# Optimization experiments

Measured on AMD Instinct MI355X. Metric: run time of the kernel, lower is better.

Reference implementation:

```python
import jax, jax.numpy as jnp
import numpy as np

K = 2  # kernel_size == stride, padding=0, dilation=1 -> non-overlapping 2x2x2 blocks


def setup_inputs() -> dict:
    key = jax.random.key(0)
    # (b, c, s, w, h) volumetric batch
    x = jax.random.normal(key, (8, 1, 64, 192, 192), dtype=jnp.float32)
    return {"x": x}


def _extract_blocks(x, k):
    # Faithful to extract_patches_3d with stride==kernel, padding=0, dilation=1:
    # the double unfold + permute + flat view yields rows ordered (b, c, do, ho, wo),
    # each row the flattened k*k*k patch.
    b, c, s, w, h = x.shape
    blk = x.reshape(b, c, s // k, k, w // k, k, h // k, k)
    blk = blk.transpose(0, 1, 2, 4, 6, 3, 5, 7)  # (b,c,do,ho,wo,k,k,k)
    return blk.reshape(-1, k * k * k)  # (N, k^3)


def reference(x):
    b, c, s, w, h = x.shape
    data = _extract_blocks(x, K)            # (N, 8)
    mean = jnp.mean(data, axis=0)           # (8,)
    centered = data - mean
    # torch.svd: data = U S V^T ; jax returns vh = V^T
    _, _, vh = jnp.linalg.svd(centered, full_matrices=False)
    pca_components = vh[:1].T               # (8, n_components=1)
    reduced = centered @ pca_components     # (N, 1)
    out = reduced.reshape(b, c, s // K, w // K, h // K)
    return out, mean, pca_components
```

## Files before the change

kernel.cpp:

```cpp
#include <hip/hip_runtime.h>

constexpr int NB     = 8 * 32 * 96 * 96;
constexpr int NPAIR  = NB / 2;
constexpr int NACC   = 44;
constexpr int GRID_A = 1024;
constexpr int TPB    = 256;
constexpr int GRID_P = 2048;

__global__ __launch_bounds__(TPB, 4)
void reduce_kernel(const float* __restrict__ x, float* __restrict__ partials,
                   unsigned int* __restrict__ ctr) {
  if (blockIdx.x == 0 && threadIdx.x == 0) *ctr = 0u;

  float acc[NACC];
#pragma unroll
  for (int i = 0; i < NACC; ++i) acc[i] = 0.0f;

  int tid = blockIdx.x * TPB + threadIdx.x;
  const int stride = GRID_A * TPB;
  for (int p = tid; p < NPAIR; p += stride) {
    int hp = p % 48;
    int t1 = p / 48;
    int wo = t1 % 96;
    int t2 = t1 / 96;
    int so = t2 % 32;
    int b  = t2 / 32;
    const float* base = x + (((b * 64 + 2 * so) * 192 + 2 * wo) * 192 + 4 * hp);
    float4 r0 = *(const float4*)(base);
    float4 r1 = *(const float4*)(base + 192);
    float4 r2 = *(const float4*)(base + 192 * 192);
    float4 r3 = *(const float4*)(base + 192 * 192 + 192);
    float v0[8] = {r0.x, r0.y, r1.x, r1.y, r2.x, r2.y, r3.x, r3.y};
    float v1[8] = {r0.z, r0.w, r1.z, r1.w, r2.z, r2.w, r3.z, r3.w};
#pragma unroll
    for (int a = 0; a < 8; ++a) acc[a] += v0[a] + v1[a];
    int k = 8;
#pragma unroll
    for (int a = 0; a < 8; ++a)
#pragma unroll
      for (int q = a; q < 8; ++q) acc[k++] += v0[a] * v0[q] + v1[a] * v1[q];
  }

#pragma unroll
  for (int i = 0; i < NACC; ++i) {
    float v = acc[i];
    for (int off = 32; off >= 1; off >>= 1) v += __shfl_down(v, off, 64);
    acc[i] = v;
  }
  __shared__ float lds[4][NACC];
  int lane = threadIdx.x & 63;
  int wv   = threadIdx.x >> 6;
  if (lane == 0) {
#pragma unroll
    for (int i = 0; i < NACC; ++i) lds[wv][i] = acc[i];
  }
  __syncthreads();
  if (threadIdx.x < NACC) {
    float s = lds[0][threadIdx.x] + lds[1][threadIdx.x] +
              lds[2][threadIdx.x] + lds[3][threadIdx.x];
    partials[threadIdx.x * GRID_A + blockIdx.x] = s;
  }
}

__device__ __forceinline__ float rdlane(float x, int lane) {
  return __int_as_float(__builtin_amdgcn_readlane(__float_as_int(x), lane));
}

template <int P, int Q>
__device__ __forceinline__ void jrot(const float (&r)[8], float& ct, float& st) {
  float app = rdlane(r[P], P);
  float aqq = rdlane(r[Q], Q);
  float apq = rdlane(r[Q], P);
  float theta = (aqq - app) * 0.5f * __builtin_amdgcn_rcpf(apq);
  float root  = __builtin_amdgcn_sqrtf(theta * theta + 1.0f);
  float tmag  = __builtin_amdgcn_rcpf(fabsf(theta) + root);
  float tt    = copysignf(tmag, theta);
  float c     = __builtin_amdgcn_rsqf(tt * tt + 1.0f);
  float s     = tt * c;
  bool zero   = (apq == 0.0f);
  ct = zero ? 1.0f : c;
  st = zero ? 0.0f : s;
}

template <int P, int Q>
__device__ __forceinline__ void jcol(float (&r)[8], float (&v)[8], float c, float s) {
  float rp = r[P], rq = r[Q];
  r[P] = c * rp - s * rq;
  r[Q] = s * rp + c * rq;
  float vp = v[P], vq = v[Q];
  v[P] = c * vp - s * vq;
  v[Q] = s * vp + c * vq;
}

template <int P0,int Q0,int P1,int Q1,int P2,int Q2,int P3,int Q3>
__device__ __forceinline__ void jacobi_round(float (&r)[8], float (&v)[8], int i) {
  float c0,s0,c1,s1,c2,s2,c3,s3;
  jrot<P0,Q0>(r, c0, s0);
  jrot<P1,Q1>(r, c1, s1);
  jrot<P2,Q2>(r, c2, s2);
  jrot<P3,Q3>(r, c3, s3);
  jcol<P0,Q0>(r, v, c0, s0);
  jcol<P1,Q1>(r, v, c1, s1);
  jcol<P2,Q2>(r, v, c2, s2);
  jcol<P3,Q3>(r, v, c3, s3);
  float alpha = 1.0f, beta = 0.0f;
  int plane = i;
  if (i == P0) { alpha = c0; beta = -s0; plane = Q0; }
  if (i == Q0) { alpha = c0; beta =  s0; plane = P0; }
  if (i == P1) { alpha = c1; beta = -s1; plane = Q1; }
  if (i == Q1) { alpha = c1; beta =  s1; plane = P1; }
  if (i == P2) { alpha = c2; beta = -s2; plane = Q2; }
  if (i == Q2) { alpha = c2; beta =  s2; plane = P2; }
  if (i == P3) { alpha = c3; beta = -s3; plane = Q3; }
  if (i == Q3) { alpha = c3; beta =  s3; plane = P3; }
  float prow[8];
#pragma unroll
  for (int j = 0; j < 8; ++j) prow[j] = __shfl(r[j], plane, 64);
#pragma unroll
  for (int j = 0; j < 8; ++j) r[j] = alpha * r[j] + beta * prow[j];
}

__global__ __launch_bounds__(TPB)
void mid_solve_kernel(const float* __restrict__ partials, double* __restrict__ sums_d,
                      unsigned int* __restrict__ ctr, float* __restrict__ res,
                      float* __restrict__ out_tail) {
  int a = blockIdx.x;
  int t = threadIdx.x;
  const float* row = partials + a * GRID_A;
  double s = (double)row[t] + (double)row[t + 256] +
             (double)row[t + 512] + (double)row[t + 768];
  for (int off = 32; off >= 1; off >>= 1) s += __shfl_down(s, off, 64);
  __shared__ double lds[4];
  __shared__ bool is_last;
  if ((t & 63) == 0) lds[t >> 6] = s;
  __syncthreads();
  if (t == 0) {
    sums_d[a] = lds[0] + lds[1] + lds[2] + lds[3];
    __threadfence();
    unsigned int old = atomicAdd(ctr, 1u);
    is_last = (old == (unsigned int)(NACC - 1));
  }
  __syncthreads();
  if (!is_last) return;
  __threadfence();

  __shared__ double sums[NACC];
  if (t < NACC) sums[t] = sums_d[t];
  __syncthreads();
  if (t >= 64) return;

  const int i = t & 7;
  const double invN = 1.0 / (double)NB;
  double mean[8];
#pragma unroll
  for (int j = 0; j < 8; ++j) mean[j] = sums[j] * invN;

  double mean_i = mean[0];
#pragma unroll
  for (int k = 1; k < 8; ++k) if (i == k) mean_i = mean[k];

  double rowd[8];
#pragma unroll
  for (int j = 0; j < 8; ++j) {
    int p = i < j ? i : j;
    int q = i < j ? j : i;
    int idx = 8 + p * 8 - (p * (p - 1)) / 2 + (q - p);
    rowd[j] = sums[idx] - (double)NB * mean_i * mean[j];
  }
  double tr = 0.0;
#pragma unroll
  for (int k = 0; k < 8; ++k) tr += __shfl(rowd[k], k, 64);
  double shift = tr * 0.125;

  float r[8], v[8];
#pragma unroll
  for (int j = 0; j < 8; ++j) {
    double d = rowd[j] - (j == i ? shift : 0.0);
    r[j] = (float)(d * (1.0 / 1536.0));
    v[j] = (j == i) ? 1.0f : 0.0f;
  }

#pragma unroll 1
  for (int sweep = 0; sweep < 6; ++sweep) {
    jacobi_round<7,0, 1,6, 2,5, 3,4>(r, v, i);
    jacobi_round<7,1, 2,0, 3,6, 4,5>(r, v, i);
    jacobi_round<7,2, 3,1, 4,0, 5,6>(r, v, i);
    jacobi_round<7,3, 4,2, 5,1, 6,0>(r, v, i);
    jacobi_round<7,4, 5,3, 6,2, 0,1>(r, v, i);
    jacobi_round<7,5, 6,4, 0,3, 1,2>(r, v, i);
    jacobi_round<7,6, 0,5, 1,4, 2,3>(r, v, i);
  }

  float diag[8];
#pragma unroll
  for (int k = 0; k < 8; ++k) diag[k] = rdlane(r[k], k);
  int best = 0; float bd = diag[0];
#pragma unroll
  for (int k = 1; k < 8; ++k) if (diag[k] > bd) { bd = diag[k]; best = k; }
  float vi = v[0];
#pragma unroll
  for (int k = 1; k < 8; ++k) if (best == k) vi = v[k];
  float vec[8];
#pragma unroll
  for (int k = 0; k < 8; ++k) vec[k] = rdlane(vi, k);
  float nrm2 = 0.0f;
#pragma unroll
  for (int k = 0; k < 8; ++k) nrm2 += vec[k] * vec[k];
  float inv = 1.0f / sqrtf(nrm2);
#pragma unroll
  for (int k = 0; k < 8; ++k) vec[k] *= inv;
  int m = 0; float am = fabsf(vec[0]);
#pragma unroll
  for (int k = 1; k < 8; ++k) { float aa = fabsf(vec[k]); if (aa > am) { am = aa; m = k; } }
  float vm = vec[0];
#pragma unroll
  for (int k = 1; k < 8; ++k) if (m == k) vm = vec[k];
  if (vm > 0.0f) {
#pragma unroll
    for (int k = 0; k < 8; ++k) vec[k] = -vec[k];
  }
  double c0d = 0.0;
#pragma unroll
  for (int k = 0; k < 8; ++k) c0d += mean[k] * (double)vec[k];

  float mi = (float)mean[0];
#pragma unroll
  for (int k = 1; k < 8; ++k) if (i == k) mi = (float)mean[k];
  float vl = vec[0];
#pragma unroll
  for (int k = 1; k < 8; ++k) if (i == k) vl = vec[k];

  if (t < 8) {
    res[t]            = vl;
    out_tail[t]       = mi;
    out_tail[8 + t]   = vl;
  }
  if (t == 0) res[8] = (float)c0d;
}

__global__ __launch_bounds__(TPB, 8)
void project_kernel(const float* __restrict__ x, const float* __restrict__ res,
                    float* __restrict__ out) {
  __shared__ float s_res[9];
  if (threadIdx.x < 9) s_res[threadIdx.x] = res[threadIdx.x];
  __syncthreads();
  float w0 = s_res[0], w1 = s_res[1], w2 = s_res[2], w3 = s_res[3];
  float w4 = s_res[4], w5 = s_res[5], w6 = s_res[6], w7 = s_res[7];
  float c0 = s_res[8];
  float2* out2 = (float2*)out;
  const int stride = GRID_P * TPB;
  for (int p = blockIdx.x * TPB + threadIdx.x; p < NPAIR; p += stride) {
    int hp = p % 48;
    int t1 = p / 48;
    int wo = t1 % 96;
    int t2 = t1 / 96;
    int so = t2 % 32;
    int b  = t2 / 32;
    const float* base = x + (((b * 64 + 2 * so) * 192 + 2 * wo) * 192 + 4 * hp);
    float4 r0 = *(const float4*)(base);
    float4 r1 = *(const float4*)(base + 192);
    float4 r2 = *(const float4*)(base + 192 * 192);
    float4 r3 = *(const float4*)(base + 192 * 192 + 192);
    float o0 = r0.x * w0 + r0.y * w1 + r1.x * w2 + r1.y * w3
             + r2.x * w4 + r2.y * w5 + r3.x * w6 + r3.y * w7 - c0;
    float o1 = r0.z * w0 + r0.w * w1 + r1.z * w2 + r1.w * w3
             + r2.z * w4 + r2.w * w5 + r3.z * w6 + r3.w * w7 - c0;
    out2[p] = make_float2(o0, o1);
  }
}

extern "C" void kernel_launch(void* const* d_in, const int* in_sizes, int n_in,
                              void* d_out, int out_size, void* d_ws, size_t ws_size,
                              hipStream_t stream) {
  (void)in_sizes; (void)n_in; (void)out_size; (void)ws_size;
  const float* x = (const float*)d_in[0];
  float* out = (float*)d_out;
  float* partials      = (float*)d_ws;
  double* sums_d       = (double*)(partials + NACC * GRID_A);
  float* res           = (float*)(sums_d + NACC);
  unsigned int* ctr    = (unsigned int*)(res + 16);

  reduce_kernel<<<GRID_A, TPB, 0, stream>>>(x, partials, ctr);
  mid_solve_kernel<<<NACC, TPB, 0, stream>>>(partials, sums_d, ctr, res, out + NB);
  project_kernel<<<GRID_P, TPB, 0, stream>>>(x, res, out);
}
```

Measured before the change: 63.59 us.

## Fuse eigen-solve into projection kernel via flag spin-wait, widen per-thread work

Merges the mid-level reduction/Jacobi solve kernel into the projection kernel. The first NACC blocks do the final sums and the last one solves the eigenproblem and sets a release flag, while every block spin-waits on that flag before projecting. This removes one kernel launch. Both the reduce and project loops now handle four blocks per thread using eight float4 loads and a float4 store, and the projection grid is halved. The spin-wait relies on all solver blocks being co-resident with the waiting blocks. With 1024 blocks at 4 per CU this is likely but not guaranteed, so there is some deadlock risk.

```diff
diff --git a/kernel.cpp b/kernel.cpp
--- a/kernel.cpp
+++ b/kernel.cpp
@@ -1,16 +1,16 @@
 #include <hip/hip_runtime.h>
 
 constexpr int NB     = 8 * 32 * 96 * 96;
-constexpr int NPAIR  = NB / 2;
+constexpr int NQUAD  = NB / 4;
 constexpr int NACC   = 44;
 constexpr int GRID_A = 1024;
 constexpr int TPB    = 256;
-constexpr int GRID_P = 2048;
+constexpr int GRID_P = 1024;
 
 __global__ __launch_bounds__(TPB, 4)
 void reduce_kernel(const float* __restrict__ x, float* __restrict__ partials,
-                   unsigned int* __restrict__ ctr) {
-  if (blockIdx.x == 0 && threadIdx.x == 0) *ctr = 0u;
+                   unsigned int* __restrict__ ctr, unsigned int* __restrict__ flag) {
+  if (blockIdx.x == 0 && threadIdx.x == 0) { *ctr = 0u; *flag = 0u; }
 
   float acc[NACC];
 #pragma unroll
@@ -18,27 +18,41 @@
 
   int tid = blockIdx.x * TPB + threadIdx.x;
   const int stride = GRID_A * TPB;
-  for (int p = tid; p < NPAIR; p += stride) {
-    int hp = p % 48;
-    int t1 = p / 48;
+  for (int q = tid; q < NQUAD; q += stride) {
+    int hq = q % 24;
+    int t1 = q / 24;
     int wo = t1 % 96;
     int t2 = t1 / 96;
     int so = t2 % 32;
     int b  = t2 / 32;
-    const float* base = x + (((b * 64 + 2 * so) * 192 + 2 * wo) * 192 + 4 * hp);
-    float4 r0 = *(const float4*)(base);
-    float4 r1 = *(const float4*)(base + 192);
-    float4 r2 = *(const float4*)(base + 192 * 192);
-    float4 r3 = *(const float4*)(base + 192 * 192 + 192);
-    float v0[8] = {r0.x, r0.y, r1.x, r1.y, r2.x, r2.y, r3.x, r3.y};
-    float v1[8] = {r0.z, r0.w, r1.z, r1.w, r2.z, r2.w, r3.z, r3.w};
-#pragma unroll
-    for (int a = 0; a < 8; ++a) acc[a] += v0[a] + v1[a];
+    const float* base = x + (((b * 64 + 2 * so) * 192 + 2 * wo) * 192 + 8 * hq);
+    float4 a0 = *(const float4*)(base);
+    float4 b0 = *(const float4*)(base + 4);
+    float4 a1 = *(const float4*)(base + 192);
+    float4 b1 = *(const float4*)(base + 196);
+    float4 a2 = *(const float4*)(base + 192 * 192);
+    float4 b2 = *(const float4*)(base + 192 * 192 + 4);
+    float4 a3 = *(const float4*)(base + 192 * 192 + 192);
+    float4 b3 = *(const float4*)(base + 192 * 192 + 196);
+    float P[4][8] = {
+      {a0.x, a0.y, a1.x, a1.y, a2.x, a2.y, a3.x, a3.y},
+      {a0.z, a0.w, a1.z, a1.w, a2.z, a2.w, a3.z, a3.w},
+      {b0.x, b0.y, b1.x, b1.y, b2.x, b2.y, b3.x, b3.y},
+      {b0.z, b0.w, b1.z, b1.w, b2.z, b2.w, b3.z, b3.w}};
+#pragma unroll
+    for (int a = 0; a < 8; ++a)
+      acc[a] += (P[0][a] + P[1][a]) + (P[2][a] + P[3][a]);
     int k = 8;
 #pragma unroll
     for (int a = 0; a < 8; ++a)
 #pragma unroll
-      for (int q = a; q < 8; ++q) acc[k++] += v0[a] * v0[q] + v1[a] * v1[q];
+      for (int c = a; c < 8; ++c) {
+        float t = P[0][a] * P[0][c];
+        t += P[1][a] * P[1][c];
+        t += P[2][a] * P[2][c];
+        t += P[3][a] * P[3][c];
+        acc[k++] += t;
+      }
   }
 
 #pragma unroll
@@ -120,152 +134,169 @@
   for (int j = 0; j < 8; ++j) r[j] = alpha * r[j] + beta * prow[j];
 }
 
-__global__ __launch_bounds__(TPB)
-void mid_solve_kernel(const float* __restrict__ partials, double* __restrict__ sums_d,
-                      unsigned int* __restrict__ ctr, float* __restrict__ res,
-                      float* __restrict__ out_tail) {
-  int a = blockIdx.x;
+__global__ __launch_bounds__(TPB, 4)
+void project_solve_kernel(const float* __restrict__ x,
+                          const float* __restrict__ partials,
+                          double* __restrict__ sums_d,
+                          unsigned int* __restrict__ ctr,
+                          unsigned int* __restrict__ flag,
+                          float* __restrict__ res,
+                          float* __restrict__ out,
+                          float* __restrict__ out_tail) {
   int t = threadIdx.x;
-  const float* row = partials + a * GRID_A;
-  double s = (double)row[t] + (double)row[t + 256] +
-             (double)row[t + 512] + (double)row[t + 768];
-  for (int off = 32; off >= 1; off >>= 1) s += __shfl_down(s, off, 64);
-  __shared__ double lds[4];
-  __shared__ bool is_last;
-  if ((t & 63) == 0) lds[t >> 6] = s;
+
+  if (blockIdx.x < NACC) {
+    const float* row = partials + blockIdx.x * GRID_A;
+    float4 u = ((const float4*)row)[t];
+    double s = (double)u.x + (double)u.y + (double)u.z + (double)u.w;
+    for (int off = 32; off >= 1; off >>= 1) s += __shfl_down(s, off, 64);
+    __shared__ double ldsd[4];
+    __shared__ bool is_last;
+    if ((t & 63) == 0) ldsd[t >> 6] = s;
+    __syncthreads();
+    if (t == 0) {
+      sums_d[blockIdx.x] = ldsd[0] + ldsd[1] + ldsd[2] + ldsd[3];
+      __threadfence();
+      unsigned int old = atomicAdd(ctr, 1u);
+      is_last = (old == (unsigned int)(NACC - 1));
+    }
+    __syncthreads();
+    if (is_last) {
+      __threadfence();
+      __shared__ double sums[NACC];
+      if (t < NACC) sums[t] = sums_d[t];
+      __syncthreads();
+      if (t < 64) {
+        const int i = t & 7;
+        const double invN = 1.0 / (double)NB;
+        double mean[8];
+#pragma unroll
+        for (int j = 0; j < 8; ++j) mean[j] = sums[j] * invN;
+        double mean_i = mean[0];
+#pragma unroll
+        for (int k = 1; k < 8; ++k) if (i == k) mean_i = mean[k];
+        double rowd[8];
+#pragma unroll
+        for (int j = 0; j < 8; ++j) {
+          int p = i < j ? i : j;
+          int q = i < j ? j : i;
+          int idx = 8 + p * 8 - (p * (p - 1)) / 2 + (q - p);
+          rowd[j] = sums[idx] - (double)NB * mean_i * mean[j];
+        }
+        double tr = 0.0;
+#pragma unroll
+        for (int k = 0; k < 8; ++k) tr += __shfl(rowd[k], k, 64);
+        double shift = tr * 0.125;
+
+        float r[8], v[8];
+#pragma unroll
+        for (int j = 0; j < 8; ++j) {
+          double d = rowd[j] - (j == i ? shift : 0.0);
+          r[j] = (float)(d * (1.0 / 1536.0));
+          v[j] = (j == i) ? 1.0f : 0.0f;
+        }
+#pragma unroll 1
+        for (int sweep = 0; sweep < 6; ++sweep) {
+          jacobi_round<7,0, 1,6, 2,5, 3,4>(r, v, i);
+          jacobi_round<7,1, 2,0, 3,6, 4,5>(r, v, i);
+          jacobi_round<7,2, 3,1, 4,0, 5,6>(r, v, i);
+          jacobi_round<7,3, 4,2, 5,1, 6,0>(r, v, i);
+          jacobi_round<7,4, 5,3, 6,2, 0,1>(r, v, i);
+          jacobi_round<7,5, 6,4, 0,3, 1,2>(r, v, i);
+          jacobi_round<7,6, 0,5, 1,4, 2,3>(r, v, i);
+        }
+        float diag[8];
+#pragma unroll
+        for (int k = 0; k < 8; ++k) diag[k] = rdlane(r[k], k);
+        int best = 0; float bd = diag[0];
+#pragma unroll
+        for (int k = 1; k < 8; ++k) if (diag[k] > bd) { bd = diag[k]; best = k; }
+        float vi = v[0];
+#pragma unroll
+        for (int k = 1; k < 8; ++k) if (best == k) vi = v[k];
+        float vec[8];
+#pragma unroll
+        for (int k = 0; k < 8; ++k) vec[k] = rdlane(vi, k);
+        float nrm2 = 0.0f;
+#pragma unroll
+        for (int k = 0; k < 8; ++k) nrm2 += vec[k] * vec[k];
+        float inv = 1.0f / sqrtf(nrm2);
+#pragma unroll
+        for (int k = 0; k < 8; ++k) vec[k] *= inv;
+        int m = 0; float am = fabsf(vec[0]);
+#pragma unroll
+        for (int k = 1; k < 8; ++k) { float aa = fabsf(vec[k]); if (aa > am) { am = aa; m = k; } }
+        float vm = vec[0];
+#pragma unroll
+        for (int k = 1; k < 8; ++k) if (m == k) vm = vec[k];
+        if (vm > 0.0f) {
+#pragma unroll
+          for (int k = 0; k < 8; ++k) vec[k] = -vec[k];
+        }
+        double c0d = 0.0;
+#pragma unroll
+        for (int k = 0; k < 8; ++k) c0d += mean[k] * (double)vec[k];
+        float mi = (float)mean[0];
+#pragma unroll
+        for (int k = 1; k < 8; ++k) if (i == k) mi = (float)mean[k];
+        float vl = vec[0];
+#pragma unroll
+        for (int k = 1; k < 8; ++k) if (i == k) vl = vec[k];
+        if (t < 8) {
+          res[t]          = vl;
+          out_tail[t]     = mi;
+          out_tail[8 + t] = vl;
+        }
+        if (t == 0) res[8] = (float)c0d;
+      }
+      __syncthreads();
+      if (t == 0) {
+        __threadfence();
+        __hip_atomic_store(flag, 1u, __ATOMIC_RELEASE, __HIP_MEMORY_SCOPE_AGENT);
+      }
+    }
+  }
+
+  __shared__ float s_res[9];
+  if (t == 0) {
+    while (__hip_atomic_load(flag, __ATOMIC_ACQUIRE, __HIP_MEMORY_SCOPE_AGENT) == 0u)
+      __builtin_amdgcn_s_sleep(2);
+  }
   __syncthreads();
-  if (t == 0) {
-    sums_d[a] = lds[0] + lds[1] + lds[2] + lds[3];
-    __threadfence();
-    unsigned int old = atomicAdd(ctr, 1u);
-    is_last = (old == (unsigned int)(NACC - 1));
-  }
+  if (t < 9)
+    s_res[t] = __hip_atomic_load(&res[t], __ATOMIC_RELAXED, __HIP_MEMORY_SCOPE_AGENT);
   __syncthreads();
-  if (!is_last) return;
-  __threadfence();
-
-  __shared__ double sums[NACC];
-  if (t < NACC) sums[t] = sums_d[t];
-  __syncthreads();
-  if (t >= 64) return;
-
-  const int i = t & 7;
-  const double invN = 1.0 / (double)NB;
-  double mean[8];
-#pragma unroll
-  for (int j = 0; j < 8; ++j) mean[j] = sums[j] * invN;
-
-  double mean_i = mean[0];
-#pragma unroll
-  for (int k = 1; k < 8; ++k) if (i == k) mean_i = mean[k];
-
-  double rowd[8];
-#pragma unroll
-  for (int j = 0; j < 8; ++j) {
-    int p = i < j ? i : j;
-    int q = i < j ? j : i;
-    int idx = 8 + p * 8 - (p * (p - 1)) / 2 + (q - p);
-    rowd[j] = sums[idx] - (double)NB * mean_i * mean[j];
-  }
-  double tr = 0.0;
-#pragma unroll
-  for (int k = 0; k < 8; ++k) tr += __shfl(rowd[k], k, 64);
-  double shift = tr * 0.125;
-
-  float r[8], v[8];
-#pragma unroll
-  for (int j = 0; j < 8; ++j) {
-    double d = rowd[j] - (j == i ? shift : 0.0);
-    r[j] = (float)(d * (1.0 / 1536.0));
-    v[j] = (j == i) ? 1.0f : 0.0f;
-  }
-
-#pragma unroll 1
-  for (int sweep = 0; sweep < 6; ++sweep) {
-    jacobi_round<7,0, 1,6, 2,5, 3,4>(r, v, i);
-    jacobi_round<7,1, 2,0, 3,6, 4,5>(r, v, i);
-    jacobi_round<7,2, 3,1, 4,0, 5,6>(r, v, i);
-    jacobi_round<7,3, 4,2, 5,1, 6,0>(r, v, i);
-    jacobi_round<7,4, 5,3, 6,2, 0,1>(r, v, i);
-    jacobi_round<7,5, 6,4, 0,3, 1,2>(r, v, i);
-    jacobi_round<7,6, 0,5, 1,4, 2,3>(r, v, i);
-  }
-
-  float diag[8];
-#pragma unroll
-  for (int k = 0; k < 8; ++k) diag[k] = rdlane(r[k], k);
-  int best = 0; float bd = diag[0];
-#pragma unroll
-  for (int k = 1; k < 8; ++k) if (diag[k] > bd) { bd = diag[k]; best = k; }
-  float vi = v[0];
-#pragma unroll
-  for (int k = 1; k < 8; ++k) if (best == k) vi = v[k];
-  float vec[8];
-#pragma unroll
-  for (int k = 0; k < 8; ++k) vec[k] = rdlane(vi, k);
-  float nrm2 = 0.0f;
-#pragma unroll
-  for (int k = 0; k < 8; ++k) nrm2 += vec[k] * vec[k];
-  float inv = 1.0f / sqrtf(nrm2);
-#pragma unroll
-  for (int k = 0; k < 8; ++k) vec[k] *= inv;
-  int m = 0; float am = fabsf(vec[0]);
-#pragma unroll
-  for (int k = 1; k < 8; ++k) { float aa = fabsf(vec[k]); if (aa > am) { am = aa; m = k; } }
-  float vm = vec[0];
-#pragma unroll
-  for (int k = 1; k < 8; ++k) if (m == k) vm = vec[k];
-  if (vm > 0.0f) {
-#pragma unroll
-    for (int k = 0; k < 8; ++k) vec[k] = -vec[k];
-  }
-  double c0d = 0.0;
-#pragma unroll
-  for (int k = 0; k < 8; ++k) c0d += mean[k] * (double)vec[k];
-
-  float mi = (float)mean[0];
-#pragma unroll
-  for (int k = 1; k < 8; ++k) if (i == k) mi = (float)mean[k];
-  float vl = vec[0];
-#pragma unroll
-  for (int k = 1; k < 8; ++k) if (i == k) vl = vec[k];
-
-  if (t < 8) {
-    res[t]            = vl;
-    out_tail[t]       = mi;
-    out_tail[8 + t]   = vl;
-  }
-  if (t == 0) res[8] = (float)c0d;
-}
-
-__global__ __launch_bounds__(TPB, 8)
-void project_kernel(const float* __restrict__ x, const float* __restrict__ res,
-                    float* __restrict__ out) {
-  __shared__ float s_res[9];
-  if (threadIdx.x < 9) s_res[threadIdx.x] = res[threadIdx.x];
-  __syncthreads();
+
   float w0 = s_res[0], w1 = s_res[1], w2 = s_res[2], w3 = s_res[3];
   float w4 = s_res[4], w5 = s_res[5], w6 = s_res[6], w7 = s_res[7];
   float c0 = s_res[8];
-  float2* out2 = (float2*)out;
+  float4* out4 = (float4*)out;
   const int stride = GRID_P * TPB;
-  for (int p = blockIdx.x * TPB + threadIdx.x; p < NPAIR; p += stride) {
-    int hp = p % 48;
-    int t1 = p / 48;
+  for (int q = blockIdx.x * TPB + t; q < NQUAD; q += stride) {
+    int hq = q % 24;
+    int t1 = q / 24;
     int wo = t1 % 96;
     int t2 = t1 / 96;
     int so = t2 % 32;
     int b  = t2 / 32;
-    const float* base = x + (((b * 64 + 2 * so) * 192 + 2 * wo) * 192 + 4 * hp);
-    float4 r0 = *(const float4*)(base);
-    float4 r1 = *(const float4*)(base + 192);
-    float4 r2 = *(const float4*)(base + 192 * 192);
-    float4 r3 = *(const float4*)(base + 192 * 192 + 192);
-    float o0 = r0.x * w0 + r0.y * w1 + r1.x * w2 + r1.y * w3
-             + r2.x * w4 + r2.y * w5 + r3.x * w6 + r3.y * w7 - c0;
-    float o1 = r0.z * w0 + r0.w * w1 + r1.z * w2 + r1.w * w3
-             + r2.z * w4 + r2.w * w5 + r3.z * w6 + r3.w * w7 - c0;
-    out2[p] = make_float2(o0, o1);
+    const float* base = x + (((b * 64 + 2 * so) * 192 + 2 * wo) * 192 + 8 * hq);
+    float4 a0 = *(const float4*)(base);
+    float4 b0 = *(const float4*)(base + 4);
+    float4 a1 = *(const float4*)(base + 192);
+    float4 b1 = *(const float4*)(base + 196);
+    float4 a2 = *(const float4*)(base + 192 * 192);
+    float4 b2 = *(const float4*)(base + 192 * 192 + 4);
+    float4 a3 = *(const float4*)(base + 192 * 192 + 192);
+    float4 b3 = *(const float4*)(base + 192 * 192 + 196);
+    float o0 = a0.x * w0 + a0.y * w1 + a1.x * w2 + a1.y * w3
+             + a2.x * w4 + a2.y * w5 + a3.x * w6 + a3.y * w7 - c0;
+    float o1 = a0.z * w0 + a0.w * w1 + a1.z * w2 + a1.w * w3
+             + a2.z * w4 + a2.w * w5 + a3.z * w6 + a3.w * w7 - c0;
+    float o2 = b0.x * w0 + b0.y * w1 + b1.x * w2 + b1.y * w3
+             + b2.x * w4 + b2.y * w5 + b3.x * w6 + b3.y * w7 - c0;
+    float o3 = b0.z * w0 + b0.w * w1 + b1.z * w2 + b1.w * w3
+             + b2.z * w4 + b2.w * w5 + b3.z * w6 + b3.w * w7 - c0;
+    out4[q] = make_float4(o0, o1, o2, o3);
   }
 }
 
@@ -275,12 +306,13 @@
   (void)in_sizes; (void)n_in; (void)out_size; (void)ws_size;
   const float* x = (const float*)d_in[0];
   float* out = (float*)d_out;
-  float* partials      = (float*)d_ws;
-  double* sums_d       = (double*)(partials + NACC * GRID_A);
-  float* res           = (float*)(sums_d + NACC);
-  unsigned int* ctr    = (unsigned int*)(res + 16);
-
-  reduce_kernel<<<GRID_A, TPB, 0, stream>>>(x, partials, ctr);
-  mid_solve_kernel<<<NACC, TPB, 0, stream>>>(partials, sums_d, ctr, res, out + NB);
-  project_kernel<<<GRID_P, TPB, 0, stream>>>(x, res, out);
-}
+  float* partials   = (float*)d_ws;
+  double* sums_d    = (double*)(partials + NACC * GRID_A);
+  float* res        = (float*)(sums_d + NACC);
+  unsigned int* ctr = (unsigned int*)(res + 16);
+  unsigned int* flg = ctr + 1;
+
+  reduce_kernel<<<GRID_A, TPB, 0, stream>>>(x, partials, ctr, flg);
+  project_solve_kernel<<<GRID_P, TPB, 0, stream>>>(x, partials, sums_d, ctr, flg,
+                                                   res, out, out + NB);
+}
```

Result: slower. 119.9 us (+88.6%).

## Fuse mid-reduction and eigen-solve into projection kernel with flag spin-wait

Applied to the files above, without the earlier changes.

Removes the separate mid_solve launch by having the first NACC blocks of the projection kernel reduce partials and, via the last-block counter, run the Jacobi eigen-solve. It then publishes the results with a release-ordered flag. All projection blocks spin on the flag before reading the weights. This aims to save a kernel launch and inter-kernel gap, at the cost of relying on co-residency of the solver blocks to avoid deadlock and on busy-waiting.

```diff
diff --git a/kernel.cpp b/kernel.cpp
--- a/kernel.cpp
+++ b/kernel.cpp
@@ -9,8 +9,8 @@
 
 __global__ __launch_bounds__(TPB, 4)
 void reduce_kernel(const float* __restrict__ x, float* __restrict__ partials,
-                   unsigned int* __restrict__ ctr) {
-  if (blockIdx.x == 0 && threadIdx.x == 0) *ctr = 0u;
+                   unsigned int* __restrict__ ctr, unsigned int* __restrict__ flag) {
+  if (blockIdx.x == 0 && threadIdx.x == 0) { *ctr = 0u; *flag = 0u; }
 
   float acc[NACC];
 #pragma unroll
@@ -120,136 +120,145 @@
   for (int j = 0; j < 8; ++j) r[j] = alpha * r[j] + beta * prow[j];
 }
 
-__global__ __launch_bounds__(TPB)
-void mid_solve_kernel(const float* __restrict__ partials, double* __restrict__ sums_d,
-                      unsigned int* __restrict__ ctr, float* __restrict__ res,
-                      float* __restrict__ out_tail) {
-  int a = blockIdx.x;
+__global__ __launch_bounds__(TPB, 8)
+void project_solve_kernel(const float* __restrict__ x,
+                          const float* __restrict__ partials,
+                          double* __restrict__ sums_d,
+                          unsigned int* __restrict__ ctr,
+                          unsigned int* __restrict__ flag,
+                          float* __restrict__ res,
+                          float* __restrict__ out,
+                          float* __restrict__ out_tail) {
   int t = threadIdx.x;
-  const float* row = partials + a * GRID_A;
-  double s = (double)row[t] + (double)row[t + 256] +
-             (double)row[t + 512] + (double)row[t + 768];
-  for (int off = 32; off >= 1; off >>= 1) s += __shfl_down(s, off, 64);
-  __shared__ double lds[4];
-  __shared__ bool is_last;
-  if ((t & 63) == 0) lds[t >> 6] = s;
+
+  if (blockIdx.x < NACC) {
+    const float* row = partials + blockIdx.x * GRID_A;
+    float4 u = ((const float4*)row)[t];
+    double s = (double)u.x + (double)u.y + (double)u.z + (double)u.w;
+    for (int off = 32; off >= 1; off >>= 1) s += __shfl_down(s, off, 64);
+    __shared__ double ldsd[4];
+    __shared__ bool is_last;
+    if ((t & 63) == 0) ldsd[t >> 6] = s;
+    __syncthreads();
+    if (t == 0) {
+      sums_d[blockIdx.x] = ldsd[0] + ldsd[1] + ldsd[2] + ldsd[3];
+      __threadfence();
+      unsigned int old = atomicAdd(ctr, 1u);
+      is_last = (old == (unsigned int)(NACC - 1));
+    }
+    __syncthreads();
+    if (is_last) {
+      __threadfence();
+      __shared__ double sums[NACC];
+      if (t < NACC) sums[t] = sums_d[t];
+      __syncthreads();
+      if (t < 64) {
+        const int i = t & 7;
+        const double invN = 1.0 / (double)NB;
+        double mean[8];
+#pragma unroll
+        for (int j = 0; j < 8; ++j) mean[j] = sums[j] * invN;
+        double mean_i = mean[0];
+#pragma unroll
+        for (int k = 1; k < 8; ++k) if (i == k) mean_i = mean[k];
+        double rowd[8];
+#pragma unroll
+        for (int j = 0; j < 8; ++j) {
+          int p = i < j ? i : j;
+          int q = i < j ? j : i;
+          int idx = 8 + p * 8 - (p * (p - 1)) / 2 + (q - p);
+          rowd[j] = sums[idx] - (double)NB * mean_i * mean[j];
+        }
+        double tr = 0.0;
+#pragma unroll
+        for (int k = 0; k < 8; ++k) tr += __shfl(rowd[k], k, 64);
+        double shift = tr * 0.125;
+
+        float r[8], v[8];
+#pragma unroll
+        for (int j = 0; j < 8; ++j) {
+          double d = rowd[j] - (j == i ? shift : 0.0);
+          r[j] = (float)(d * (1.0 / 1536.0));
+          v[j] = (j == i) ? 1.0f : 0.0f;
+        }
+#pragma unroll 1
+        for (int sweep = 0; sweep < 6; ++sweep) {
+          jacobi_round<7,0, 1,6, 2,5, 3,4>(r, v, i);
+          jacobi_round<7,1, 2,0, 3,6, 4,5>(r, v, i);
+          jacobi_round<7,2, 3,1, 4,0, 5,6>(r, v, i);
+          jacobi_round<7,3, 4,2, 5,1, 6,0>(r, v, i);
+          jacobi_round<7,4, 5,3, 6,2, 0,1>(r, v, i);
+          jacobi_round<7,5, 6,4, 0,3, 1,2>(r, v, i);
+          jacobi_round<7,6, 0,5, 1,4, 2,3>(r, v, i);
+        }
+        float diag[8];
+#pragma unroll
+        for (int k = 0; k < 8; ++k) diag[k] = rdlane(r[k], k);
+        int best = 0; float bd = diag[0];
+#pragma unroll
+        for (int k = 1; k < 8; ++k) if (diag[k] > bd) { bd = diag[k]; best = k; }
+        float vi = v[0];
+#pragma unroll
+        for (int k = 1; k < 8; ++k) if (best == k) vi = v[k];
+        float vec[8];
+#pragma unroll
+        for (int k = 0; k < 8; ++k) vec[k] = rdlane(vi, k);
+        float nrm2 = 0.0f;
+#pragma unroll
+        for (int k = 0; k < 8; ++k) nrm2 += vec[k] * vec[k];
+        float inv = 1.0f / sqrtf(nrm2);
+#pragma unroll
+        for (int k = 0; k < 8; ++k) vec[k] *= inv;
+        int m = 0; float am = fabsf(vec[0]);
+#pragma unroll
+        for (int k = 1; k < 8; ++k) { float aa = fabsf(vec[k]); if (aa > am) { am = aa; m = k; } }
+        float vm = vec[0];
+#pragma unroll
+        for (int k = 1; k < 8; ++k) if (m == k) vm = vec[k];
+        if (vm > 0.0f) {
+#pragma unroll
+          for (int k = 0; k < 8; ++k) vec[k] = -vec[k];
+        }
+        double c0d = 0.0;
+#pragma unroll
+        for (int k = 0; k < 8; ++k) c0d += mean[k] * (double)vec[k];
+        float mi = (float)mean[0];
+#pragma unroll
+        for (int k = 1; k < 8; ++k) if (i == k) mi = (float)mean[k];
+        float vl = vec[0];
+#pragma unroll
+        for (int k = 1; k < 8; ++k) if (i == k) vl = vec[k];
+        if (t < 8) {
+          res[t]          = vl;
+          out_tail[t]     = mi;
+          out_tail[8 + t] = vl;
+        }
+        if (t == 0) res[8] = (float)c0d;
+      }
+      __syncthreads();
+      if (t == 0) {
+        __threadfence();
+        __hip_atomic_store(flag, 1u, __ATOMIC_RELEASE, __HIP_MEMORY_SCOPE_AGENT);
+      }
+    }
+  }
+
+  __shared__ float s_res[9];
+  if (t == 0) {
+    while (__hip_atomic_load(flag, __ATOMIC_RELAXED, __HIP_MEMORY_SCOPE_AGENT) == 0u)
+      __builtin_amdgcn_s_sleep(8);
+  }
   __syncthreads();
-  if (t == 0) {
-    sums_d[a] = lds[0] + lds[1] + lds[2] + lds[3];
-    __threadfence();
-    unsigned int old = atomicAdd(ctr, 1u);
-    is_last = (old == (unsigned int)(NACC - 1));
-  }
+  if (t < 9)
+    s_res[t] = __hip_atomic_load(&res[t], __ATOMIC_RELAXED, __HIP_MEMORY_SCOPE_AGENT);
   __syncthreads();
-  if (!is_last) return;
-  __threadfence();
-
-  __shared__ double sums[NACC];
-  if (t < NACC) sums[t] = sums_d[t];
-  __syncthreads();
-  if (t >= 64) return;
-
-  const int i = t & 7;
-  const double invN = 1.0 / (double)NB;
-  double mean[8];
-#pragma unroll
-  for (int j = 0; j < 8; ++j) mean[j] = sums[j] * invN;
-
-  double mean_i = mean[0];
-#pragma unroll
-  for (int k = 1; k < 8; ++k) if (i == k) mean_i = mean[k];
-
-  double rowd[8];
-#pragma unroll
-  for (int j = 0; j < 8; ++j) {
-    int p = i < j ? i : j;
-    int q = i < j ? j : i;
-    int idx = 8 + p * 8 - (p * (p - 1)) / 2 + (q - p);
-    rowd[j] = sums[idx] - (double)NB * mean_i * mean[j];
-  }
-  double tr = 0.0;
-#pragma unroll
-  for (int k = 0; k < 8; ++k) tr += __shfl(rowd[k], k, 64);
-  double shift = tr * 0.125;
-
-  float r[8], v[8];
-#pragma unroll
-  for (int j = 0; j < 8; ++j) {
-    double d = rowd[j] - (j == i ? shift : 0.0);
-    r[j] = (float)(d * (1.0 / 1536.0));
-    v[j] = (j == i) ? 1.0f : 0.0f;
-  }
-
-#pragma unroll 1
-  for (int sweep = 0; sweep < 6; ++sweep) {
-    jacobi_round<7,0, 1,6, 2,5, 3,4>(r, v, i);
-    jacobi_round<7,1, 2,0, 3,6, 4,5>(r, v, i);
-    jacobi_round<7,2, 3,1, 4,0, 5,6>(r, v, i);
-    jacobi_round<7,3, 4,2, 5,1, 6,0>(r, v, i);
-    jacobi_round<7,4, 5,3, 6,2, 0,1>(r, v, i);
-    jacobi_round<7,5, 6,4, 0,3, 1,2>(r, v, i);
-    jacobi_round<7,6, 0,5, 1,4, 2,3>(r, v, i);
-  }
-
-  float diag[8];
-#pragma unroll
-  for (int k = 0; k < 8; ++k) diag[k] = rdlane(r[k], k);
-  int best = 0; float bd = diag[0];
-#pragma unroll
-  for (int k = 1; k < 8; ++k) if (diag[k] > bd) { bd = diag[k]; best = k; }
-  float vi = v[0];
-#pragma unroll
-  for (int k = 1; k < 8; ++k) if (best == k) vi = v[k];
-  float vec[8];
-#pragma unroll
-  for (int k = 0; k < 8; ++k) vec[k] = rdlane(vi, k);
-  float nrm2 = 0.0f;
-#pragma unroll
-  for (int k = 0; k < 8; ++k) nrm2 += vec[k] * vec[k];
-  float inv = 1.0f / sqrtf(nrm2);
-#pragma unroll
-  for (int k = 0; k < 8; ++k) vec[k] *= inv;
-  int m = 0; float am = fabsf(vec[0]);
-#pragma unroll
-  for (int k = 1; k < 8; ++k) { float aa = fabsf(vec[k]); if (aa > am) { am = aa; m = k; } }
-  float vm = vec[0];
-#pragma unroll
-  for (int k = 1; k < 8; ++k) if (m == k) vm = vec[k];
-  if (vm > 0.0f) {
-#pragma unroll
-    for (int k = 0; k < 8; ++k) vec[k] = -vec[k];
-  }
-  double c0d = 0.0;
-#pragma unroll
-  for (int k = 0; k < 8; ++k) c0d += mean[k] * (double)vec[k];
-
-  float mi = (float)mean[0];
-#pragma unroll
-  for (int k = 1; k < 8; ++k) if (i == k) mi = (float)mean[k];
-  float vl = vec[0];
-#pragma unroll
-  for (int k = 1; k < 8; ++k) if (i == k) vl = vec[k];
-
-  if (t < 8) {
-    res[t]            = vl;
-    out_tail[t]       = mi;
-    out_tail[8 + t]   = vl;
-  }
-  if (t == 0) res[8] = (float)c0d;
-}
-
-__global__ __launch_bounds__(TPB, 8)
-void project_kernel(const float* __restrict__ x, const float* __restrict__ res,
-                    float* __restrict__ out) {
-  __shared__ float s_res[9];
-  if (threadIdx.x < 9) s_res[threadIdx.x] = res[threadIdx.x];
-  __syncthreads();
+
   float w0 = s_res[0], w1 = s_res[1], w2 = s_res[2], w3 = s_res[3];
   float w4 = s_res[4], w5 = s_res[5], w6 = s_res[6], w7 = s_res[7];
   float c0 = s_res[8];
   float2* out2 = (float2*)out;
   const int stride = GRID_P * TPB;
-  for (int p = blockIdx.x * TPB + threadIdx.x; p < NPAIR; p += stride) {
+  for (int p = blockIdx.x * TPB + t; p < NPAIR; p += stride) {
     int hp = p % 48;
     int t1 = p / 48;
     int wo = t1 % 96;
@@ -275,12 +284,13 @@
   (void)in_sizes; (void)n_in; (void)out_size; (void)ws_size;
   const float* x = (const float*)d_in[0];
   float* out = (float*)d_out;
-  float* partials      = (float*)d_ws;
-  double* sums_d       = (double*)(partials + NACC * GRID_A);
-  float* res           = (float*)(sums_d + NACC);
-  unsigned int* ctr    = (unsigned int*)(res + 16);
-
-  reduce_kernel<<<GRID_A, TPB, 0, stream>>>(x, partials, ctr);
-  mid_solve_kernel<<<NACC, TPB, 0, stream>>>(partials, sums_d, ctr, res, out + NB);
-  project_kernel<<<GRID_P, TPB, 0, stream>>>(x, res, out);
-}
+  float* partials   = (float*)d_ws;
+  double* sums_d    = (double*)(partials + NACC * GRID_A);
+  float* res        = (float*)(sums_d + NACC);
+  unsigned int* ctr = (unsigned int*)(res + 16);
+  unsigned int* flg = ctr + 1;
+
+  reduce_kernel<<<GRID_A, TPB, 0, stream>>>(x, partials, ctr, flg);
+  project_solve_kernel<<<GRID_P, TPB, 0, stream>>>(x, partials, sums_d, ctr, flg,
+                                                   res, out, out + NB);
+}
```

Measured after the change: 74.00 us. 1.16x slower.
